# Performance work log

Measured on AMD Instinct MI355X. Metric: run time of the kernel, lower is better.

## Reference

```python
import jax, jax.numpy as jnp
import numpy as np

N = 100000
E = 3200000
F_IN = 128
H1 = 16
H2 = 8
NEG_SLOPE = 0.2


def _gat_layer(x, src, dst, W, a_src, a_dst, b, n_nodes):
    # x: [N, Fin]; src/dst: [E_tot] (self-loops included); W: [Fin, Fout]
    h = x @ W                                   # [N, Fout]
    e_src = h @ a_src                           # [N]
    e_dst = h @ a_dst                           # [N]
    e = e_src[src] + e_dst[dst]                 # [E_tot]
    e = jnp.where(e > 0, e, NEG_SLOPE * e)      # leaky_relu(0.2)
    m = jax.ops.segment_max(e, dst, num_segments=n_nodes)   # [N]
    w = jnp.exp(e - m[dst])                     # [E_tot]
    s = jax.ops.segment_sum(w, dst, num_segments=n_nodes)   # [N]
    alpha = w / s[dst]                          # [E_tot]
    out = jax.ops.segment_sum(alpha[:, None] * h[src], dst, num_segments=n_nodes)
    return out + b


def setup_inputs() -> dict:
    key = jax.random.key(0)
    ks = jax.random.split(key, 12)
    x = jax.random.normal(ks[0], (N, F_IN), dtype=jnp.float32)
    edge_index = jax.random.randint(ks[1], (E, 2), 0, N, dtype=jnp.int64)
    s1 = 1.0 / np.sqrt(F_IN)
    s2 = 1.0 / np.sqrt(H1)
    s3 = 1.0 / np.sqrt(H2)
    return {
        "x": x,
        "edge_index": edge_index,
        "W1": jax.random.normal(ks[2], (F_IN, H1), dtype=jnp.float32) * s1,
        "a1_src": jax.random.normal(ks[3], (H1,), dtype=jnp.float32) * s2,
        "a1_dst": jax.random.normal(ks[4], (H1,), dtype=jnp.float32) * s2,
        "b1": jnp.zeros((H1,), dtype=jnp.float32),
        "W2": jax.random.normal(ks[5], (H1, H2), dtype=jnp.float32) * s2,
        "a2_src": jax.random.normal(ks[6], (H2,), dtype=jnp.float32) * s3,
        "a2_dst": jax.random.normal(ks[7], (H2,), dtype=jnp.float32) * s3,
        "b2": jnp.zeros((H2,), dtype=jnp.float32),
        "Wf": jax.random.normal(ks[8], (H2, 1), dtype=jnp.float32) * s3,
        "bf": jnp.zeros((1,), dtype=jnp.float32),
    }


def reference(x, edge_index, W1, a1_src, a1_dst, b1, W2, a2_src, a2_dst, b2, Wf, bf):
    ei = edge_index.T                            # [2, E] as in original forward
    loop = jnp.arange(N, dtype=ei.dtype)
    src = jnp.concatenate([ei[0], loop])         # PyG add_self_loops=True
    dst = jnp.concatenate([ei[1], loop])
    h = jax.nn.relu(_gat_layer(x, src, dst, W1, a1_src, a1_dst, b1, N))
    # dropout p=0.05 is identity at inference
    h = jax.nn.relu(_gat_layer(h, src, dst, W2, a2_src, a2_dst, b2, N))
    return h @ Wf + bf                           # [N, 1]
```

## Files before the change

### kernel.cpp

```cpp
#include <hip/hip_runtime.h>
#include <math.h>

#define N_NODES 100000
#define N_EDGES 3200000
#define E_TOT   (N_EDGES + N_NODES)
#define F_IN    128
#define H1      16
#define H2      8
#define NEG     0.2f
#define LOG2E   1.4426950408889634f
#define NBUCKET ((N_NODES + 255) >> 8)
#define NCHUNK  512
#define CE      ((N_EDGES + NCHUNK - 1) / NCHUNK)

typedef _Float16 half2v __attribute__((ext_vector_type(2)));
typedef _Float16 half8v __attribute__((ext_vector_type(8)));

__global__ __launch_bounds__(256) void k1_xw(
        const float* __restrict__ x, const float* __restrict__ W1,
        const float* __restrict__ a1s, const float* __restrict__ a1d,
        char* __restrict__ g1, float* __restrict__ e1d) {
    __shared__ float w1s[F_IN * H1];
    __shared__ float xs[16 * 132];
    __shared__ float a1ss[H1], a1ds[H1];
    const int tid = threadIdx.x;
    for (int i = tid; i < F_IN * H1; i += 256) w1s[i] = W1[i];
    if (tid < H1) { a1ss[tid] = a1s[tid]; a1ds[tid] = a1d[tid]; }
    const int rowbase = blockIdx.x * 16;
    #pragma unroll
    for (int i = 0; i < 2; i++) {
        int q = tid + i * 256;
        int r = q >> 5, c = q & 31;
        float4 v = *(const float4*)(x + (size_t)(rowbase + r) * F_IN + c * 4);
        *(float4*)(xs + r * 132 + c * 4) = v;
    }
    __syncthreads();
    const int g = tid >> 4, j = tid & 15;
    const float* xrow = xs + g * 132;
    float acc = 0.f;
    #pragma unroll 8
    for (int k = 0; k < F_IN; k++) acc += xrow[k] * w1s[k * H1 + j];
    const int row = rowbase + g;
    char* grow = g1 + (size_t)row * 64;
    ((_Float16*)grow)[j] = (_Float16)acc;
    float ps = acc * a1ss[j];
    float pd = acc * a1ds[j];
    #pragma unroll
    for (int m = 8; m >= 1; m >>= 1) {
        ps += __shfl_xor(ps, m, 16);
        pd += __shfl_xor(pd, m, 16);
    }
    if (j == 0) { *(float*)(grow + 32) = ps * LOG2E; e1d[row] = pd * LOG2E; }
}


__global__ __launch_bounds__(256) void k_count(const int2* __restrict__ ei,
                                               int* __restrict__ counts) {
    __shared__ int hist[NBUCKET];
    for (int i = threadIdx.x; i < NBUCKET; i += 256) hist[i] = 0;
    __syncthreads();
    const int b = blockIdx.x;
    const int beg = b * CE, end = min(N_EDGES, beg + CE);
    for (int e = beg + threadIdx.x; e < end; e += 256)
        atomicAdd(&hist[ei[e].y >> 8], 1);
    __syncthreads();
    for (int i = threadIdx.x; i < NBUCKET; i += 256)
        counts[i * NCHUNK + b] = hist[i];
}

__global__ __launch_bounds__(512) void k_scanA(int* __restrict__ counts,
                                               int* __restrict__ btot) {
    __shared__ int lds[NCHUNK];
    const int k = blockIdx.x, t = threadIdx.x;
    int v = counts[k * NCHUNK + t];
    lds[t] = v;
    __syncthreads();
    for (int off = 1; off < NCHUNK; off <<= 1) {
        int u = (t >= off) ? lds[t - off] : 0;
        __syncthreads();
        lds[t] += u;
        __syncthreads();
    }
    counts[k * NCHUNK + t] = lds[t] - v;
    if (t == NCHUNK - 1) btot[k] = lds[t];
}

__global__ __launch_bounds__(512) void k_scanB(const int* __restrict__ btot,
                                               int* __restrict__ bbase) {
    __shared__ int lds[512];
    const int t = threadIdx.x;
    int v = (t < NBUCKET) ? btot[t] : 0;
    lds[t] = v;
    __syncthreads();
    for (int off = 1; off < 512; off <<= 1) {
        int u = (t >= off) ? lds[t - off] : 0;
        __syncthreads();
        lds[t] += u;
        __syncthreads();
    }
    if (t < NBUCKET) bbase[t] = lds[t] - v;
    if (t == 511) bbase[NBUCKET] = lds[511];
}

__global__ __launch_bounds__(256) void k_reorder(const int2* __restrict__ ei,
                                                 const int* __restrict__ counts,
                                                 const int* __restrict__ bbase,
                                                 int* __restrict__ pairs) {
    __shared__ int cur[NBUCKET];
    const int b = blockIdx.x;
    for (int i = threadIdx.x; i < NBUCKET; i += 256)
        cur[i] = bbase[i] + counts[i * NCHUNK + b];
    __syncthreads();
    const int beg = b * CE, end = min(N_EDGES, beg + CE);
    for (int e = beg + threadIdx.x; e < end; e += 256) {
        int2 v = ei[e];
        int k = v.y >> 8;
        int pos = atomicAdd(&cur[k], 1);
        pairs[pos] = (v.x << 8) | (v.y & 255);
    }
}

__global__ __launch_bounds__(256) void k_csr(const int* __restrict__ pairs,
                                             const int* __restrict__ bbase,
                                             int* __restrict__ rowg,
                                             int* __restrict__ degg,
                                             int* __restrict__ sorted_src) {
    __shared__ int deg[256], scn[256], cur[256];
    const int k = blockIdx.x, t = threadIdx.x;
    const int n0 = k << 8;
    const int nn = min(256, N_NODES - n0);
    deg[t] = 0;
    __syncthreads();
    const int ebeg = bbase[k], eend = bbase[k + 1];
    for (int e = ebeg + t; e < eend; e += 256)
        atomicAdd(&deg[pairs[e] & 255], 1);
    __syncthreads();
    int v = (t < nn) ? deg[t] : 0;
    scn[t] = v;
    __syncthreads();
    for (int off = 1; off < 256; off <<= 1) {
        int u = (t >= off) ? scn[t - off] : 0;
        __syncthreads();
        scn[t] += u;
        __syncthreads();
    }
    int excl = scn[t] - v;
    if (t < nn) {
        int r = ebeg + excl + n0 + t;
        rowg[n0 + t] = r;
        degg[n0 + t] = v + 1;
        sorted_src[r] = n0 + t;
        cur[t] = r + 1;
    }
    __syncthreads();
    for (int e = ebeg + t; e < eend; e += 256) {
        int p = pairs[e];
        int pos = atomicAdd(&cur[p & 255], 1);
        sorted_src[pos] = p >> 8;
    }
}

template <int LPN, int U, int ROWB, int ESOFF, bool LAYER2>
__global__ __launch_bounds__(256) void k_agg(
        const int* __restrict__ row, const int* __restrict__ deg,
        const int* __restrict__ sorted_src,
        const float* __restrict__ ed, const char* __restrict__ gtab,
        const float* __restrict__ b,
        const float* __restrict__ W2, const float* __restrict__ a2s,
        const float* __restrict__ a2d,
        char* __restrict__ g2out, float* __restrict__ e2d_out,
        const float* __restrict__ Wf, const float* __restrict__ bf,
        float* __restrict__ out) {
    __shared__ float w2s[H1 * H2];
    __shared__ float a2ss[H2], a2ds[H2];
    if (!LAYER2) {
        for (int i = threadIdx.x; i < H1 * H2; i += 256) w2s[i] = W2[i];
        if (threadIdx.x < H2) { a2ss[threadIdx.x] = a2s[threadIdx.x];
                                a2ds[threadIdx.x] = a2d[threadIdx.x]; }
        __syncthreads();
    }
    const int sub = threadIdx.x & (LPN - 1);
    const int node = (blockIdx.x * 256 + threadIdx.x) / LPN;
    if (node >= N_NODES) return;
    const int beg = row[node];
    const int cnt = deg[node];
    const float edv = ed[node];
    float2 acc = make_float2(0.f, 0.f);
    float s = 0.f;
    int srcs[U];
    #pragma unroll
    for (int i = 0; i < U; i++) srcs[i] = sorted_src[beg + (i < cnt ? i : 0)];
    for (int t0 = 0; t0 < cnt; t0 += U) {
        float evs[U];
        half2v hvs[U];
        #pragma unroll
        for (int i = 0; i < U; i++) {
            const char* rp = gtab + (unsigned)srcs[i] * ROWB;
            hvs[i] = *(const half2v*)(rp + sub * 4);
            evs[i] = *(const float*)(rp + ESOFF);
        }
        int nsrcs[U];
        #pragma unroll
        for (int i = 0; i < U; i++) {
            int idx = t0 + U + i;
            nsrcs[i] = sorted_src[beg + (idx < cnt ? idx : 0)];
        }
        #pragma unroll
        for (int i = 0; i < U; i++) {
            if (t0 + i < cnt) {
                float k = evs[i] + edv;
                k = fmaxf(k, NEG * k);
                float p = __builtin_amdgcn_exp2f(k);
                s += p;
                acc.x += p * (float)hvs[i].x;
                acc.y += p * (float)hvs[i].y;
            }
        }
        #pragma unroll
        for (int i = 0; i < U; i++) srcs[i] = nsrcs[i];
    }
    const float inv = 1.f / s;
    const float2 bv = ((const float2*)b)[sub];
    float2 o;
    o.x = fmaxf(acc.x * inv + bv.x, 0.f);
    o.y = fmaxf(acc.y * inv + bv.y, 0.f);
    if (!LAYER2) {
        float p2[H2];
        const float* w0 = w2s + (2 * sub) * H2;
        const float* w1 = w2s + (2 * sub + 1) * H2;
        #pragma unroll
        for (int i = 0; i < H2; i++) p2[i] = o.x * w0[i] + o.y * w1[i];
        #pragma unroll
        for (int i = 0; i < H2; i++) {
            p2[i] += __shfl_xor(p2[i], 1);
            p2[i] += __shfl_xor(p2[i], 2);
            p2[i] += __shfl_xor(p2[i], 4);
        }
        float es2 = 0.f, ed2 = 0.f;
        #pragma unroll
        for (int i = 0; i < H2; i++) { es2 += p2[i] * a2ss[i]; ed2 += p2[i] * a2ds[i]; }
        char* orow = g2out + (size_t)node * 32;
        if (sub == 0) {
            half8v h8;
            #pragma unroll
            for (int i = 0; i < H2; i++) h8[i] = (_Float16)p2[i];
            *(half8v*)orow = h8;
        } else if (sub == 1) {
            *(float*)(orow + 16) = es2 * LOG2E;
        } else if (sub == 2) {
            e2d_out[node] = ed2 * LOG2E;
        }
    } else {
        const float2 wv = ((const float2*)Wf)[sub];
        float r = o.x * wv.x + o.y * wv.y;
        r += __shfl_xor(r, 1);
        r += __shfl_xor(r, 2);
        if (sub == 0) out[node] = r + bf[0];
    }
}

extern "C" void kernel_launch(void* const* d_in, const int* in_sizes, int n_in,
                              void* d_out, int out_size, void* d_ws, size_t ws_size,
                              hipStream_t stream) {
    const float* x    = (const float*)d_in[0];
    const int2*  ei   = (const int2*)d_in[1];
    const float* W1   = (const float*)d_in[2];
    const float* a1s  = (const float*)d_in[3];
    const float* a1d  = (const float*)d_in[4];
    const float* b1   = (const float*)d_in[5];
    const float* W2   = (const float*)d_in[6];
    const float* a2s  = (const float*)d_in[7];
    const float* a2d  = (const float*)d_in[8];
    const float* b2   = (const float*)d_in[9];
    const float* Wf   = (const float*)d_in[10];
    const float* bf   = (const float*)d_in[11];
    float* out = (float*)d_out;

    char* wp = (char*)d_ws;
    int* sorted_src = (int*)wp;   wp += sizeof(int) * (size_t)E_TOT;
    char* pairs_region = wp;      wp += sizeof(int) * (size_t)N_EDGES;
    int* counts     = (int*)wp;   wp += sizeof(int) * (size_t)NBUCKET * NCHUNK;
    int* btot       = (int*)wp;   wp += sizeof(int) * (NBUCKET + 1);
    int* bbase      = (int*)wp;   wp += sizeof(int) * (NBUCKET + 1);
    int* degg       = (int*)wp;   wp += sizeof(int) * N_NODES;
    int* rowg       = (int*)wp;   wp += sizeof(int) * N_NODES;
    char* g1        = wp;         wp += (size_t)64 * N_NODES;
    float* e1d      = (float*)wp; wp += sizeof(float) * N_NODES;

    int*   pairs = (int*)pairs_region;
    char*  g2    = pairs_region;
    float* e2d   = (float*)(g2 + (size_t)32 * N_NODES);

    k_count<<<NCHUNK, 256, 0, stream>>>(ei, counts);
    k_scanA<<<NBUCKET, 512, 0, stream>>>(counts, btot);
    k_scanB<<<1, 512, 0, stream>>>(btot, bbase);
    k_reorder<<<NCHUNK, 256, 0, stream>>>(ei, counts, bbase, pairs);
    k_csr<<<NBUCKET, 256, 0, stream>>>(pairs, bbase, rowg, degg, sorted_src);
    k1_xw<<<N_NODES / 16, 256, 0, stream>>>(x, W1, a1s, a1d, g1, e1d);
    k_agg<8, 16, 64, 32, false><<<(N_NODES * 8 + 255) / 256, 256, 0, stream>>>(
        rowg, degg, sorted_src, e1d, g1, b1, W2, a2s, a2d, g2, e2d,
        nullptr, nullptr, nullptr);
    k_agg<4, 16, 32, 16, true><<<(N_NODES * 4 + 255) / 256, 256, 0, stream>>>(
        rowg, degg, sorted_src, e2d, g2, b2, nullptr, nullptr, nullptr,
        nullptr, nullptr, Wf, bf, out);
}
```

Baseline: 268.6 us.

## Replace two-level bucket sort CSR build with global-atomic degree count and fill

The CSR construction no longer uses a two-pass bucketed counting sort with LDS histograms (count, reorder into pairs, per-bucket CSR). It now counts per-node degrees with global atomics, scans them, and scatters each edge's source directly into its slot via a global atomic cursor. This drops the intermediate pairs array and one full pass over the edges, but adds millions of contended global atomics with random access, and the order of sources within a row becomes nondeterministic.

```diff
diff --git a/kernel.cpp b/kernel.cpp
--- a/kernel.cpp
+++ b/kernel.cpp
@@ -10,8 +10,6 @@
 #define NEG     0.2f
 #define LOG2E   1.4426950408889634f
 #define NBUCKET ((N_NODES + 255) >> 8)
-#define NCHUNK  512
-#define CE      ((N_EDGES + NCHUNK - 1) / NCHUNK)
 
 typedef _Float16 half2v __attribute__((ext_vector_type(2)));
 typedef _Float16 half8v __attribute__((ext_vector_type(8)));
@@ -54,35 +52,30 @@
 }
 
 
-__global__ __launch_bounds__(256) void k_count(const int2* __restrict__ ei,
-                                               int* __restrict__ counts) {
-    __shared__ int hist[NBUCKET];
-    for (int i = threadIdx.x; i < NBUCKET; i += 256) hist[i] = 0;
-    __syncthreads();
-    const int b = blockIdx.x;
-    const int beg = b * CE, end = min(N_EDGES, beg + CE);
-    for (int e = beg + threadIdx.x; e < end; e += 256)
-        atomicAdd(&hist[ei[e].y >> 8], 1);
-    __syncthreads();
-    for (int i = threadIdx.x; i < NBUCKET; i += 256)
-        counts[i * NCHUNK + b] = hist[i];
-}
-
-__global__ __launch_bounds__(512) void k_scanA(int* __restrict__ counts,
+__global__ __launch_bounds__(256) void k_deg(const int2* __restrict__ ei,
+                                             int* __restrict__ deg) {
+    const int stride = gridDim.x * 256;
+    for (int e = blockIdx.x * 256 + threadIdx.x; e < N_EDGES; e += stride)
+        atomicAdd(&deg[ei[e].y], 1);
+}
+
+__global__ __launch_bounds__(256) void k_scanA(const int* __restrict__ deg,
+                                               int* __restrict__ scn,
                                                int* __restrict__ btot) {
-    __shared__ int lds[NCHUNK];
-    const int k = blockIdx.x, t = threadIdx.x;
-    int v = counts[k * NCHUNK + t];
+    __shared__ int lds[256];
+    const int b = blockIdx.x, t = threadIdx.x;
+    const int n = b * 256 + t;
+    int v = (n < N_NODES) ? deg[n] : 0;
     lds[t] = v;
     __syncthreads();
-    for (int off = 1; off < NCHUNK; off <<= 1) {
+    for (int off = 1; off < 256; off <<= 1) {
         int u = (t >= off) ? lds[t - off] : 0;
         __syncthreads();
         lds[t] += u;
         __syncthreads();
     }
-    counts[k * NCHUNK + t] = lds[t] - v;
-    if (t == NCHUNK - 1) btot[k] = lds[t];
+    if (n < N_NODES) scn[n] = lds[t] - v;
+    if (t == 255) btot[b] = lds[255];
 }
 
 __global__ __launch_bounds__(512) void k_scanB(const int* __restrict__ btot,
@@ -102,61 +95,30 @@
     if (t == 511) bbase[NBUCKET] = lds[511];
 }
 
-__global__ __launch_bounds__(256) void k_reorder(const int2* __restrict__ ei,
-                                                 const int* __restrict__ counts,
-                                                 const int* __restrict__ bbase,
-                                                 int* __restrict__ pairs) {
-    __shared__ int cur[NBUCKET];
-    const int b = blockIdx.x;
-    for (int i = threadIdx.x; i < NBUCKET; i += 256)
-        cur[i] = bbase[i] + counts[i * NCHUNK + b];
-    __syncthreads();
-    const int beg = b * CE, end = min(N_EDGES, beg + CE);
-    for (int e = beg + threadIdx.x; e < end; e += 256) {
-        int2 v = ei[e];
-        int k = v.y >> 8;
-        int pos = atomicAdd(&cur[k], 1);
-        pairs[pos] = (v.x << 8) | (v.y & 255);
-    }
-}
-
-__global__ __launch_bounds__(256) void k_csr(const int* __restrict__ pairs,
+__global__ __launch_bounds__(256) void k_fin(const int* __restrict__ deg,
+                                             const int* __restrict__ scn,
                                              const int* __restrict__ bbase,
                                              int* __restrict__ rowg,
                                              int* __restrict__ degg,
+                                             int* __restrict__ cur,
                                              int* __restrict__ sorted_src) {
-    __shared__ int deg[256], scn[256], cur[256];
-    const int k = blockIdx.x, t = threadIdx.x;
-    const int n0 = k << 8;
-    const int nn = min(256, N_NODES - n0);
-    deg[t] = 0;
-    __syncthreads();
-    const int ebeg = bbase[k], eend = bbase[k + 1];
-    for (int e = ebeg + t; e < eend; e += 256)
-        atomicAdd(&deg[pairs[e] & 255], 1);
-    __syncthreads();
-    int v = (t < nn) ? deg[t] : 0;
-    scn[t] = v;
-    __syncthreads();
-    for (int off = 1; off < 256; off <<= 1) {
-        int u = (t >= off) ? scn[t - off] : 0;
-        __syncthreads();
-        scn[t] += u;
-        __syncthreads();
-    }
-    int excl = scn[t] - v;
-    if (t < nn) {
-        int r = ebeg + excl + n0 + t;
-        rowg[n0 + t] = r;
-        degg[n0 + t] = v + 1;
-        sorted_src[r] = n0 + t;
-        cur[t] = r + 1;
-    }
-    __syncthreads();
-    for (int e = ebeg + t; e < eend; e += 256) {
-        int p = pairs[e];
-        int pos = atomicAdd(&cur[p & 255], 1);
-        sorted_src[pos] = p >> 8;
+    const int n = blockIdx.x * 256 + threadIdx.x;
+    if (n >= N_NODES) return;
+    const int r = bbase[n >> 8] + scn[n] + n;
+    rowg[n] = r;
+    degg[n] = deg[n] + 1;
+    sorted_src[r] = n;
+    cur[n] = r + 1;
+}
+
+__global__ __launch_bounds__(256) void k_fill(const int2* __restrict__ ei,
+                                              int* __restrict__ cur,
+                                              int* __restrict__ sorted_src) {
+    const int stride = gridDim.x * 256;
+    for (int e = blockIdx.x * 256 + threadIdx.x; e < N_EDGES; e += stride) {
+        int2 v = ei[e];
+        int pos = atomicAdd(&cur[v.y], 1);
+        sorted_src[pos] = v.x;
     }
 }
 
@@ -277,25 +239,25 @@
     float* out = (float*)d_out;
 
     char* wp = (char*)d_ws;
-    int* sorted_src = (int*)wp;   wp += sizeof(int) * (size_t)E_TOT;
-    char* pairs_region = wp;      wp += sizeof(int) * (size_t)N_EDGES;
-    int* counts     = (int*)wp;   wp += sizeof(int) * (size_t)NBUCKET * NCHUNK;
-    int* btot       = (int*)wp;   wp += sizeof(int) * (NBUCKET + 1);
-    int* bbase      = (int*)wp;   wp += sizeof(int) * (NBUCKET + 1);
-    int* degg       = (int*)wp;   wp += sizeof(int) * N_NODES;
-    int* rowg       = (int*)wp;   wp += sizeof(int) * N_NODES;
-    char* g1        = wp;         wp += (size_t)64 * N_NODES;
-    float* e1d      = (float*)wp; wp += sizeof(float) * N_NODES;
-
-    int*   pairs = (int*)pairs_region;
-    char*  g2    = pairs_region;
-    float* e2d   = (float*)(g2 + (size_t)32 * N_NODES);
-
-    k_count<<<NCHUNK, 256, 0, stream>>>(ei, counts);
-    k_scanA<<<NBUCKET, 512, 0, stream>>>(counts, btot);
+    int*   sorted_src = (int*)wp;   wp += sizeof(int) * (size_t)E_TOT;
+    int*   deg        = (int*)wp;   wp += sizeof(int) * N_NODES;
+    int*   scn        = (int*)wp;   wp += sizeof(int) * N_NODES;
+    int*   cur        = (int*)wp;   wp += sizeof(int) * N_NODES;
+    int*   degg       = (int*)wp;   wp += sizeof(int) * N_NODES;
+    int*   rowg       = (int*)wp;   wp += sizeof(int) * N_NODES;
+    int*   btot       = (int*)wp;   wp += sizeof(int) * (NBUCKET + 1);
+    int*   bbase      = (int*)wp;   wp += sizeof(int) * (NBUCKET + 1);
+    char*  g1         = wp;         wp += (size_t)64 * N_NODES;
+    float* e1d        = (float*)wp; wp += sizeof(float) * N_NODES;
+    char*  g2         = wp;         wp += (size_t)32 * N_NODES;
+    float* e2d        = (float*)wp; wp += sizeof(float) * N_NODES;
+
+    hipMemsetAsync(deg, 0, sizeof(int) * N_NODES, stream);
+    k_deg<<<2048, 256, 0, stream>>>(ei, deg);
+    k_scanA<<<NBUCKET, 256, 0, stream>>>(deg, scn, btot);
     k_scanB<<<1, 512, 0, stream>>>(btot, bbase);
-    k_reorder<<<NCHUNK, 256, 0, stream>>>(ei, counts, bbase, pairs);
-    k_csr<<<NBUCKET, 256, 0, stream>>>(pairs, bbase, rowg, degg, sorted_src);
+    k_fin<<<NBUCKET, 256, 0, stream>>>(deg, scn, bbase, rowg, degg, cur, sorted_src);
+    k_fill<<<2048, 256, 0, stream>>>(ei, cur, sorted_src);
     k1_xw<<<N_NODES / 16, 256, 0, stream>>>(x, W1, a1s, a1d, g1, e1d);
     k_agg<8, 16, 64, 32, false><<<(N_NODES * 8 + 255) / 256, 256, 0, stream>>>(
         rowg, degg, sorted_src, e1d, g1, b1, W2, a2s, a2d, g2, e2d,
```

Result: slower. 599.9 us (+123.3%).

## Fuse edge histogram into XW kernel and drop the separate bucket-scan kernel

Applied to the files above, without the earlier changes.

The edge-count histogram blocks are merged into the x@W1 projection kernel as extra blocks, so the two independent workloads share one launch and can overlap. The single-block bucket-base scan kernel is removed: k_reorder recomputes the bucket prefix in shared memory, and k_csr gets its base through a block reduction over btot. Edge loads are widened to int4, two edges per load. The cost is redundant scan work in every reorder and csr block, plus shared-memory use in the fused kernel that can lower occupancy for the XW blocks. The vectorised loops assume CE is even and the chunk offsets stay 16-byte aligned, which holds for these sizes.

```diff
diff --git a/kernel.cpp b/kernel.cpp
--- a/kernel.cpp
+++ b/kernel.cpp
@@ -16,17 +16,34 @@
 typedef _Float16 half2v __attribute__((ext_vector_type(2)));
 typedef _Float16 half8v __attribute__((ext_vector_type(8)));
 
-__global__ __launch_bounds__(256) void k1_xw(
+__global__ __launch_bounds__(256) void k1_count(
         const float* __restrict__ x, const float* __restrict__ W1,
         const float* __restrict__ a1s, const float* __restrict__ a1d,
-        char* __restrict__ g1, float* __restrict__ e1d) {
+        char* __restrict__ g1, float* __restrict__ e1d,
+        const int2* __restrict__ ei, int* __restrict__ counts) {
+    __shared__ int hist[NBUCKET];
     __shared__ float w1s[F_IN * H1];
     __shared__ float xs[16 * 132];
     __shared__ float a1ss[H1], a1ds[H1];
     const int tid = threadIdx.x;
+    if (blockIdx.x < NCHUNK) {
+        for (int i = tid; i < NBUCKET; i += 256) hist[i] = 0;
+        __syncthreads();
+        const int b = blockIdx.x;
+        const int4* p4 = (const int4*)(ei + b * CE);
+        for (int q = tid; q < CE / 2; q += 256) {
+            int4 v = p4[q];
+            atomicAdd(&hist[v.y >> 8], 1);
+            atomicAdd(&hist[v.w >> 8], 1);
+        }
+        __syncthreads();
+        for (int i = tid; i < NBUCKET; i += 256)
+            counts[i * NCHUNK + b] = hist[i];
+        return;
+    }
     for (int i = tid; i < F_IN * H1; i += 256) w1s[i] = W1[i];
     if (tid < H1) { a1ss[tid] = a1s[tid]; a1ds[tid] = a1d[tid]; }
-    const int rowbase = blockIdx.x * 16;
+    const int rowbase = (blockIdx.x - NCHUNK) * 16;
     #pragma unroll
     for (int i = 0; i < 2; i++) {
         int q = tid + i * 256;
@@ -53,21 +70,6 @@
     if (j == 0) { *(float*)(grow + 32) = ps * LOG2E; e1d[row] = pd * LOG2E; }
 }
 
-
-__global__ __launch_bounds__(256) void k_count(const int2* __restrict__ ei,
-                                               int* __restrict__ counts) {
-    __shared__ int hist[NBUCKET];
-    for (int i = threadIdx.x; i < NBUCKET; i += 256) hist[i] = 0;
-    __syncthreads();
-    const int b = blockIdx.x;
-    const int beg = b * CE, end = min(N_EDGES, beg + CE);
-    for (int e = beg + threadIdx.x; e < end; e += 256)
-        atomicAdd(&hist[ei[e].y >> 8], 1);
-    __syncthreads();
-    for (int i = threadIdx.x; i < NBUCKET; i += 256)
-        counts[i * NCHUNK + b] = hist[i];
-}
-
 __global__ __launch_bounds__(512) void k_scanA(int* __restrict__ counts,
                                                int* __restrict__ btot) {
     __shared__ int lds[NCHUNK];
@@ -85,53 +87,64 @@
     if (t == NCHUNK - 1) btot[k] = lds[t];
 }
 
-__global__ __launch_bounds__(512) void k_scanB(const int* __restrict__ btot,
-                                               int* __restrict__ bbase) {
-    __shared__ int lds[512];
-    const int t = threadIdx.x;
-    int v = (t < NBUCKET) ? btot[t] : 0;
-    lds[t] = v;
-    __syncthreads();
-    for (int off = 1; off < 512; off <<= 1) {
-        int u = (t >= off) ? lds[t - off] : 0;
-        __syncthreads();
-        lds[t] += u;
-        __syncthreads();
-    }
-    if (t < NBUCKET) bbase[t] = lds[t] - v;
-    if (t == 511) bbase[NBUCKET] = lds[511];
-}
-
 __global__ __launch_bounds__(256) void k_reorder(const int2* __restrict__ ei,
                                                  const int* __restrict__ counts,
-                                                 const int* __restrict__ bbase,
+                                                 const int* __restrict__ btot,
                                                  int* __restrict__ pairs) {
+    __shared__ int bb[512];
+    __shared__ int ps[256];
     __shared__ int cur[NBUCKET];
-    const int b = blockIdx.x;
-    for (int i = threadIdx.x; i < NBUCKET; i += 256)
-        cur[i] = bbase[i] + counts[i * NCHUNK + b];
-    __syncthreads();
-    const int beg = b * CE, end = min(N_EDGES, beg + CE);
-    for (int e = beg + threadIdx.x; e < end; e += 256) {
-        int2 v = ei[e];
-        int k = v.y >> 8;
-        int pos = atomicAdd(&cur[k], 1);
-        pairs[pos] = (v.x << 8) | (v.y & 255);
+    const int b = blockIdx.x, tid = threadIdx.x;
+    bb[tid]       = (tid < NBUCKET) ? btot[tid] : 0;
+    bb[tid + 256] = (tid + 256 < NBUCKET) ? btot[tid + 256] : 0;
+    __syncthreads();
+    const int lo = bb[2 * tid], hi = bb[2 * tid + 1];
+    ps[tid] = lo + hi;
+    __syncthreads();
+    for (int off = 1; off < 256; off <<= 1) {
+        int u = (tid >= off) ? ps[tid - off] : 0;
+        __syncthreads();
+        ps[tid] += u;
+        __syncthreads();
+    }
+    const int ep = ps[tid] - (lo + hi);
+    __syncthreads();
+    bb[2 * tid]     = ep;
+    bb[2 * tid + 1] = ep + lo;
+    __syncthreads();
+    for (int i = tid; i < NBUCKET; i += 256)
+        cur[i] = bb[i] + counts[i * NCHUNK + b];
+    __syncthreads();
+    const int4* p4 = (const int4*)(ei + b * CE);
+    for (int q = tid; q < CE / 2; q += 256) {
+        int4 v = p4[q];
+        int pos0 = atomicAdd(&cur[v.y >> 8], 1);
+        pairs[pos0] = (v.x << 8) | (v.y & 255);
+        int pos1 = atomicAdd(&cur[v.w >> 8], 1);
+        pairs[pos1] = (v.z << 8) | (v.w & 255);
     }
 }
 
 __global__ __launch_bounds__(256) void k_csr(const int* __restrict__ pairs,
-                                             const int* __restrict__ bbase,
+                                             const int* __restrict__ btot,
                                              int* __restrict__ rowg,
                                              int* __restrict__ degg,
                                              int* __restrict__ sorted_src) {
-    __shared__ int deg[256], scn[256], cur[256];
+    __shared__ int deg[256], scn[256], cur[256], red[256];
     const int k = blockIdx.x, t = threadIdx.x;
     const int n0 = k << 8;
     const int nn = min(256, N_NODES - n0);
+    int part = 0;
+    for (int i = t; i < k; i += 256) part += btot[i];
+    red[t] = part;
     deg[t] = 0;
     __syncthreads();
-    const int ebeg = bbase[k], eend = bbase[k + 1];
+    for (int off = 128; off >= 1; off >>= 1) {
+        if (t < off) red[t] += red[t + off];
+        __syncthreads();
+    }
+    const int ebeg = red[0];
+    const int eend = ebeg + btot[k];
     for (int e = ebeg + t; e < eend; e += 256)
         atomicAdd(&deg[pairs[e] & 255], 1);
     __syncthreads();
@@ -281,7 +294,6 @@
     char* pairs_region = wp;      wp += sizeof(int) * (size_t)N_EDGES;
     int* counts     = (int*)wp;   wp += sizeof(int) * (size_t)NBUCKET * NCHUNK;
     int* btot       = (int*)wp;   wp += sizeof(int) * (NBUCKET + 1);
-    int* bbase      = (int*)wp;   wp += sizeof(int) * (NBUCKET + 1);
     int* degg       = (int*)wp;   wp += sizeof(int) * N_NODES;
     int* rowg       = (int*)wp;   wp += sizeof(int) * N_NODES;
     char* g1        = wp;         wp += (size_t)64 * N_NODES;
@@ -291,12 +303,11 @@
     char*  g2    = pairs_region;
     float* e2d   = (float*)(g2 + (size_t)32 * N_NODES);
 
-    k_count<<<NCHUNK, 256, 0, stream>>>(ei, counts);
+    k1_count<<<NCHUNK + N_NODES / 16, 256, 0, stream>>>(
+        x, W1, a1s, a1d, g1, e1d, ei, counts);
     k_scanA<<<NBUCKET, 512, 0, stream>>>(counts, btot);
-    k_scanB<<<1, 512, 0, stream>>>(btot, bbase);
-    k_reorder<<<NCHUNK, 256, 0, stream>>>(ei, counts, bbase, pairs);
-    k_csr<<<NBUCKET, 256, 0, stream>>>(pairs, bbase, rowg, degg, sorted_src);
-    k1_xw<<<N_NODES / 16, 256, 0, stream>>>(x, W1, a1s, a1d, g1, e1d);
+    k_reorder<<<NCHUNK, 256, 0, stream>>>(ei, counts, btot, pairs);
+    k_csr<<<NBUCKET, 256, 0, stream>>>(pairs, btot, rowg, degg, sorted_src);
     k_agg<8, 16, 64, 32, false><<<(N_NODES * 8 + 255) / 256, 256, 0, stream>>>(
         rowg, degg, sorted_src, e1d, g1, b1, W2, a2s, a2d, g2, e2d,
         nullptr, nullptr, nullptr);
```

Measured after the change: 269.8 us. No clear change (+0.4%).
